# Kernel tuning notes

Hardware: AMD Instinct MI355X
Metric: run time of the kernel (lower is better)

The kernel has to match this reference:

```python
import jax, jax.numpy as jnp
import numpy as np

MARGIN = 0.3
EPS = 1e-12  # guards sqrt at zero distance (diagonal)


def setup_inputs() -> dict:
    key = jax.random.key(0)
    k1, k2 = jax.random.split(key)
    features = jax.random.normal(k1, (8192, 256), dtype=jnp.float32)
    labels = jax.random.randint(k2, (8192,), 0, 512, dtype=jnp.int64)
    return {"features": features, "labels": labels}


def reference(features, labels):
    # L2 normalize rows (F.normalize default: p=2, dim=1, eps=1e-12)
    norm = jnp.linalg.norm(features, axis=1, keepdims=True)
    f = features / jnp.maximum(norm, 1e-12)

    # pairwise euclidean distances: ||a||^2 + ||b||^2 - 2 a.b, then sqrt
    sq = jnp.sum(f * f, axis=1)  # [N]
    gram = f @ f.T               # [N, N]
    d2 = sq[:, None] + sq[None, :] - 2.0 * gram
    dist = jnp.sqrt(jnp.clip(d2, EPS))  # [N, N]

    mask_pos = labels[:, None] == labels[None, :]  # includes diagonal, as in torch code

    hardest_pos = jnp.max(dist * mask_pos.astype(dist.dtype), axis=1)
    dist_neg = jnp.where(mask_pos, jnp.inf, dist)
    hardest_neg = jnp.min(dist_neg, axis=1)

    loss = jax.nn.relu(hardest_pos - hardest_neg + MARGIN)
    return jnp.mean(loss)
```

## Files before the change

kernel.cpp:

```cpp
#include <hip/hip_runtime.h>
#include <hip/hip_bf16.h>
#include <hip/hip_fp8.h>
#include <math.h>

#define N 8192
#define D 256
#define MARGIN 0.3f
#define EPS 1e-12f

#define BT 128
#define NJB (N / BT)
#define TOTAL_TRI (NJB * (NJB + 1) / 2)

typedef __attribute__((ext_vector_type(4))) float floatx4;
typedef long long fp8x8;
typedef __attribute__((ext_vector_type(2))) long long llx2;

static __device__ inline unsigned char f2fp8(float f) {
    __hip_fp8_e4m3 h(f);
    return *reinterpret_cast<unsigned char*>(&h);
}


__global__ __launch_bounds__(256) void normalize_kernel(const float* __restrict__ x,
                                                        unsigned char* __restrict__ fn8t,
                                                        float* __restrict__ out) {
    __shared__ unsigned char lnorm[16][256];
    const int g    = blockIdx.x;
    const int t    = threadIdx.x;
    const int w    = t >> 6;
    const int lane = t & 63;
    if (g == 0 && t == 0) out[0] = 0.0f;

    #pragma unroll
    for (int rr = 0; rr < 4; rr++) {
        const int rl  = w * 4 + rr;
        const int row = g * 16 + rl;
        float4 v = ((const float4*)(x + (size_t)row * D))[lane];
        float s = v.x * v.x + v.y * v.y + v.z * v.z + v.w * v.w;
        #pragma unroll
        for (int off = 32; off; off >>= 1) s += __shfl_down(s, off);
        s = __shfl(s, 0);
        const float inv = 1.0f / fmaxf(sqrtf(s), 1e-12f);
        uchar4 b;
        b.x = f2fp8(v.x * inv); b.y = f2fp8(v.y * inv);
        b.z = f2fp8(v.z * inv); b.w = f2fp8(v.w * inv);
        *(uchar4*)(&lnorm[rl][lane * 4]) = b;
    }
    __syncthreads();
    const int kk = t >> 5;
    const int pp = (t & 31) * 2;
    unsigned char* base = fn8t + (size_t)g * 4096 + (kk >> 1) * 1024 + (kk & 1) * 8;
    #pragma unroll
    for (int e = 0; e < 2; e++) {
        const int p    = pp + e;
        const int quad = p >> 4;
        const int l15  = p & 15;
        *(fp8x8*)(base + p * 16) = *(const fp8x8*)(&lnorm[l15][kk * 32 + quad * 8]);
    }
}

__global__ __launch_bounds__(256, 3) void gram_kernel(const unsigned char* __restrict__ fn8t,
                                                      const int* __restrict__ lab,
                                                      float* __restrict__ gp_part,
                                                      float* __restrict__ gn_part) {
    __shared__ float rT[4][BT][17];
    __shared__ float cGp[BT][2], cGn[BT][2];

    const int bidx = blockIdx.x;
    const int idx  = (bidx & 7) * 260 + (bidx >> 3);
    const float c = 2.0f * NJB + 1.0f;
    int ib = (int)((c - sqrtf(c * c - 8.0f * (float)idx)) * 0.5f);
    while (ib > 0 && idx < ib * NJB - ib * (ib - 1) / 2) ib--;
    while (idx >= (ib + 1) * NJB - (ib + 1) * ib / 2) ib++;
    const int jb = ib + (idx - (ib * NJB - ib * (ib - 1) / 2));
    const bool offdiag = (jb > ib);
    const int i0 = ib * BT, j0 = jb * BT;

    const int t    = threadIdx.x;
    const int w    = t >> 6;
    const int lane = t & 63;
    const int wi   = w >> 1, wj = w & 1;
    const int quad = lane >> 4;
    const int l15  = lane & 15;

    const unsigned char* pA[4];
    const unsigned char* pB[4];
    #pragma unroll
    for (int m = 0; m < 4; m++)
        pA[m] = fn8t + ((size_t)(ib * 8 + wi * 4 + m)) * 4096 + lane * 16;
    #pragma unroll
    for (int n = 0; n < 4; n++)
        pB[n] = fn8t + ((size_t)(jb * 8 + wj * 4 + n)) * 4096 + lane * 16;

    floatx4 acc[4][4];
    #pragma unroll
    for (int m = 0; m < 4; m++)
        #pragma unroll
        for (int n = 0; n < 4; n++)
            acc[m][n] = (floatx4){0.f, 0.f, 0.f, 0.f};

    #pragma unroll
    for (int P = 0; P < 4; P++) {
        llx2 a2[4], b2[4];
        #pragma unroll
        for (int m = 0; m < 4; m++) a2[m] = *(const llx2*)(pA[m] + P * 1024);
        #pragma unroll
        for (int n = 0; n < 4; n++) b2[n] = *(const llx2*)(pB[n] + P * 1024);
        #pragma unroll
        for (int m = 0; m < 4; m++)
            #pragma unroll
            for (int n = 0; n < 4; n++)
                acc[m][n] = __builtin_amdgcn_mfma_f32_16x16x32_fp8_fp8(a2[m][0], b2[n][0], acc[m][n], 0, 0, 0);
        #pragma unroll
        for (int m = 0; m < 4; m++)
            #pragma unroll
            for (int n = 0; n < 4; n++)
                acc[m][n] = __builtin_amdgcn_mfma_f32_16x16x32_fp8_fp8(a2[m][1], b2[n][1], acc[m][n], 0, 0, 0);
    }

    int labj[4];
    #pragma unroll
    for (int n = 0; n < 4; n++) labj[n] = lab[j0 + wj * 64 + n * 16 + l15];
    float gpc[4], gnc[4];
    #pragma unroll
    for (int n = 0; n < 4; n++) { gpc[n] = INFINITY; gnc[n] = -INFINITY; }

    #pragma unroll
    for (int m = 0; m < 4; m++) {
        const int4 li4 = *(const int4*)(lab + i0 + wi * 64 + m * 16 + quad * 4);
        const int labi[4] = {li4.x, li4.y, li4.z, li4.w};
        #pragma unroll
        for (int r = 0; r < 4; r++) {
            float pr = INFINITY, nr = -INFINITY;
            #pragma unroll
            for (int n = 0; n < 4; n++) {
                const float g = acc[m][n][r];
                const bool same = (labi[r] == labj[n]);
                const float selp = same ? g : INFINITY;
                const float seln = same ? -INFINITY : g;
                pr = fminf(pr, selp);           nr = fmaxf(nr, seln);
                gpc[n] = fminf(gpc[n], selp);   gnc[n] = fmaxf(gnc[n], seln);
            }
            if (offdiag) {
                const int irow = wi * 64 + m * 16 + quad * 4 + r;
                rT[(wj << 1) + 0][irow][l15] = pr;
                rT[(wj << 1) + 1][irow][l15] = nr;
            }
        }
    }
    #pragma unroll
    for (int n = 0; n < 4; n++) {
        float p = gpc[n], q2 = gnc[n];
        p  = fminf(p,  __shfl_xor(p, 16));  p  = fminf(p,  __shfl_xor(p, 32));
        q2 = fmaxf(q2, __shfl_xor(q2, 16)); q2 = fmaxf(q2, __shfl_xor(q2, 32));
        if (quad == 0) {
            const int col = wj * 64 + n * 16 + l15;
            cGp[col][wi] = p; cGn[col][wi] = q2;
        }
    }
    __syncthreads();
    if (t < BT) {
        gp_part[(size_t)ib * N + j0 + t] = fminf(cGp[t][0], cGp[t][1]);
        gn_part[(size_t)ib * N + j0 + t] = fmaxf(cGn[t][0], cGn[t][1]);
    } else if (offdiag) {
        const int i = t - BT;
        float p = INFINITY, nn = -INFINITY;
        #pragma unroll
        for (int k = 0; k < 16; k++) {
            p  = fminf(p,  fminf(rT[0][i][k], rT[2][i][k]));
            nn = fmaxf(nn, fmaxf(rT[1][i][k], rT[3][i][k]));
        }
        gp_part[(size_t)jb * N + i0 + i] = p;
        gn_part[(size_t)jb * N + i0 + i] = nn;
    }
}

__global__ __launch_bounds__(256) void reduce_kernel(const float* __restrict__ gp_part,
                                                     const float* __restrict__ gn_part,
                                                     float* __restrict__ out) {
    __shared__ float redp[32][5], redn[32][5];
    const int t  = threadIdx.x;
    const int r  = blockIdx.x * 32 + (t & 31);
    const int sg = t >> 5;
    float gp = INFINITY, gn = -INFINITY;
    #pragma unroll
    for (int q = 0; q < 8; q++) {
        const int s = sg * 8 + q;
        gp = fminf(gp, gp_part[(size_t)s * N + r]);
        gn = fmaxf(gn, gn_part[(size_t)s * N + r]);
    }
    gp = fminf(gp, __shfl_xor(gp, 32));
    gn = fmaxf(gn, __shfl_xor(gn, 32));
    const int w = t >> 6;
    if ((t & 63) < 32) { redp[t & 31][w] = gp; redn[t & 31][w] = gn; }
    __syncthreads();
    if (t < 32) {
        const float p  = fminf(fminf(redp[t][0], redp[t][1]), fminf(redp[t][2], redp[t][3]));
        const float nn = fmaxf(fmaxf(redn[t][0], redn[t][1]), fmaxf(redn[t][2], redn[t][3]));
        const float dp = sqrtf(fmaxf(2.0f - 2.0f * p,  EPS));
        const float dn = sqrtf(fmaxf(2.0f - 2.0f * nn, EPS));
        const float l  = dp - dn + MARGIN;
        float sum = (l > 0.0f) ? l : 0.0f;
        #pragma unroll
        for (int off = 16; off; off >>= 1) sum += __shfl_down(sum, off);
        if (t == 0) atomicAdd(out, sum * (1.0f / (float)N));
    }
}

extern "C" void kernel_launch(void* const* d_in, const int* in_sizes, int n_in,
                              void* d_out, int out_size, void* d_ws, size_t ws_size,
                              hipStream_t stream) {
    const float* x   = (const float*)d_in[0];
    const int*   lab = (const int*)d_in[1];
    float* out = (float*)d_out;

    char* ws = (char*)d_ws;
    unsigned char* fn8t = (unsigned char*)ws;
    float* gp_part = (float*)(ws + (size_t)N * D);
    float* gn_part = gp_part + (size_t)NJB * N;

    normalize_kernel<<<N / 16, 256, 0, stream>>>(x, fn8t, out);
    gram_kernel<<<TOTAL_TRI, 256, 0, stream>>>(fn8t, lab, gp_part, gn_part);
    reduce_kernel<<<N / 32, 256, 0, stream>>>(gp_part, gn_part, out);
}
```

Baseline: 88.21 us.

## Switch gram kernel to 32x32x16 fp8 MFMA with matching fp8 layout

Replaces the 4x4 grid of 16x16x32 fp8 MFMA tiles per wave with a 2x2 grid of 32x32x16 MFMA tiles. The normalize kernel now writes the packed fp8 operands in a 32-row-group layout to match. The epilogue row/column reductions are reworked for the 32x32 accumulator layout, adding a shuffle before the shared-memory row writes. Launch bounds are raised to 4 blocks per SM to improve occupancy. The larger MFMA tile is meant to cut the number of operand loads and instructions per block, at the cost of a more complex epilogue.

```diff
diff --git a/kernel.cpp b/kernel.cpp
--- a/kernel.cpp
+++ b/kernel.cpp
@@ -12,7 +12,7 @@
 #define NJB (N / BT)
 #define TOTAL_TRI (NJB * (NJB + 1) / 2)
 
-typedef __attribute__((ext_vector_type(4))) float floatx4;
+typedef __attribute__((ext_vector_type(16))) float floatx16;
 typedef long long fp8x8;
 typedef __attribute__((ext_vector_type(2))) long long llx2;
 
@@ -25,17 +25,17 @@
 __global__ __launch_bounds__(256) void normalize_kernel(const float* __restrict__ x,
                                                         unsigned char* __restrict__ fn8t,
                                                         float* __restrict__ out) {
-    __shared__ unsigned char lnorm[16][256];
-    const int g    = blockIdx.x;
+    __shared__ unsigned char lnorm[32][256];
+    const int G    = blockIdx.x;
     const int t    = threadIdx.x;
     const int w    = t >> 6;
     const int lane = t & 63;
-    if (g == 0 && t == 0) out[0] = 0.0f;
-
-    #pragma unroll
-    for (int rr = 0; rr < 4; rr++) {
-        const int rl  = w * 4 + rr;
-        const int row = g * 16 + rl;
+    if (G == 0 && t == 0) out[0] = 0.0f;
+
+    #pragma unroll
+    for (int rr = 0; rr < 8; rr++) {
+        const int rl  = w * 8 + rr;
+        const int row = G * 32 + rl;
         float4 v = ((const float4*)(x + (size_t)row * D))[lane];
         float s = v.x * v.x + v.y * v.y + v.z * v.z + v.w * v.w;
         #pragma unroll
@@ -48,19 +48,17 @@
         *(uchar4*)(&lnorm[rl][lane * 4]) = b;
     }
     __syncthreads();
-    const int kk = t >> 5;
-    const int pp = (t & 31) * 2;
-    unsigned char* base = fn8t + (size_t)g * 4096 + (kk >> 1) * 1024 + (kk & 1) * 8;
-    #pragma unroll
-    for (int e = 0; e < 2; e++) {
-        const int p    = pp + e;
-        const int quad = p >> 4;
-        const int l15  = p & 15;
-        *(fp8x8*)(base + p * 16) = *(const fp8x8*)(&lnorm[l15][kk * 32 + quad * 8]);
-    }
-}
-
-__global__ __launch_bounds__(256, 3) void gram_kernel(const unsigned char* __restrict__ fn8t,
+    const int s  = t >> 4;
+    const int p0 = (t & 15) * 4;
+    unsigned char* base = fn8t + (size_t)G * 8192 + (s >> 1) * 1024 + (s & 1) * 8;
+    #pragma unroll
+    for (int e = 0; e < 4; e++) {
+        const int p = p0 + e;
+        *(fp8x8*)(base + p * 16) = *(const fp8x8*)(&lnorm[p & 31][s * 16 + (p >> 5) * 8]);
+    }
+}
+
+__global__ __launch_bounds__(256, 4) void gram_kernel(const unsigned char* __restrict__ fn8t,
                                                       const int* __restrict__ lab,
                                                       float* __restrict__ gp_part,
                                                       float* __restrict__ gn_part) {
@@ -81,81 +79,89 @@
     const int w    = t >> 6;
     const int lane = t & 63;
     const int wi   = w >> 1, wj = w & 1;
-    const int quad = lane >> 4;
-    const int l15  = lane & 15;
-
-    const unsigned char* pA[4];
-    const unsigned char* pB[4];
-    #pragma unroll
-    for (int m = 0; m < 4; m++)
-        pA[m] = fn8t + ((size_t)(ib * 8 + wi * 4 + m)) * 4096 + lane * 16;
-    #pragma unroll
-    for (int n = 0; n < 4; n++)
-        pB[n] = fn8t + ((size_t)(jb * 8 + wj * 4 + n)) * 4096 + lane * 16;
-
-    floatx4 acc[4][4];
-    #pragma unroll
-    for (int m = 0; m < 4; m++)
-        #pragma unroll
-        for (int n = 0; n < 4; n++)
-            acc[m][n] = (floatx4){0.f, 0.f, 0.f, 0.f};
-
-    #pragma unroll
-    for (int P = 0; P < 4; P++) {
-        llx2 a2[4], b2[4];
-        #pragma unroll
-        for (int m = 0; m < 4; m++) a2[m] = *(const llx2*)(pA[m] + P * 1024);
-        #pragma unroll
-        for (int n = 0; n < 4; n++) b2[n] = *(const llx2*)(pB[n] + P * 1024);
-        #pragma unroll
-        for (int m = 0; m < 4; m++)
+    const int l31  = lane & 31;
+    const int hi   = lane >> 5;
+
+    const unsigned char* pA[2];
+    const unsigned char* pB[2];
+    #pragma unroll
+    for (int m = 0; m < 2; m++)
+        pA[m] = fn8t + ((size_t)(ib * 4 + wi * 2 + m)) * 8192 + lane * 16;
+    #pragma unroll
+    for (int n = 0; n < 2; n++)
+        pB[n] = fn8t + ((size_t)(jb * 4 + wj * 2 + n)) * 8192 + lane * 16;
+
+    floatx16 acc[2][2];
+    #pragma unroll
+    for (int m = 0; m < 2; m++)
+        #pragma unroll
+        for (int n = 0; n < 2; n++)
+            acc[m][n] = (floatx16)(0.0f);
+
+    #pragma unroll
+    for (int P = 0; P < 8; P++) {
+        llx2 a2[2], b2[2];
+        #pragma unroll
+        for (int m = 0; m < 2; m++) a2[m] = *(const llx2*)(pA[m] + P * 1024);
+        #pragma unroll
+        for (int n = 0; n < 2; n++) b2[n] = *(const llx2*)(pB[n] + P * 1024);
+        #pragma unroll
+        for (int m = 0; m < 2; m++)
             #pragma unroll
-            for (int n = 0; n < 4; n++)
-                acc[m][n] = __builtin_amdgcn_mfma_f32_16x16x32_fp8_fp8(a2[m][0], b2[n][0], acc[m][n], 0, 0, 0);
-        #pragma unroll
-        for (int m = 0; m < 4; m++)
+            for (int n = 0; n < 2; n++)
+                acc[m][n] = __builtin_amdgcn_mfma_f32_32x32x16_fp8_fp8(a2[m][0], b2[n][0], acc[m][n], 0, 0, 0);
+        #pragma unroll
+        for (int m = 0; m < 2; m++)
             #pragma unroll
-            for (int n = 0; n < 4; n++)
-                acc[m][n] = __builtin_amdgcn_mfma_f32_16x16x32_fp8_fp8(a2[m][1], b2[n][1], acc[m][n], 0, 0, 0);
-    }
-
-    int labj[4];
-    #pragma unroll
-    for (int n = 0; n < 4; n++) labj[n] = lab[j0 + wj * 64 + n * 16 + l15];
-    float gpc[4], gnc[4];
-    #pragma unroll
-    for (int n = 0; n < 4; n++) { gpc[n] = INFINITY; gnc[n] = -INFINITY; }
-
-    #pragma unroll
-    for (int m = 0; m < 4; m++) {
-        const int4 li4 = *(const int4*)(lab + i0 + wi * 64 + m * 16 + quad * 4);
-        const int labi[4] = {li4.x, li4.y, li4.z, li4.w};
-        #pragma unroll
-        for (int r = 0; r < 4; r++) {
-            float pr = INFINITY, nr = -INFINITY;
+            for (int n = 0; n < 2; n++)
+                acc[m][n] = __builtin_amdgcn_mfma_f32_32x32x16_fp8_fp8(a2[m][1], b2[n][1], acc[m][n], 0, 0, 0);
+    }
+
+    int labj[2];
+    #pragma unroll
+    for (int n = 0; n < 2; n++) labj[n] = lab[j0 + wj * 64 + n * 32 + l31];
+    float gpc[2], gnc[2];
+    #pragma unroll
+    for (int n = 0; n < 2; n++) { gpc[n] = INFINITY; gnc[n] = -INFINITY; }
+
+    #pragma unroll
+    for (int m = 0; m < 2; m++) {
+        #pragma unroll
+        for (int q = 0; q < 4; q++) {
+            const int4 li4 = *(const int4*)(lab + i0 + wi * 64 + m * 32 + q * 8 + hi * 4);
+            const int labi[4] = {li4.x, li4.y, li4.z, li4.w};
             #pragma unroll
-            for (int n = 0; n < 4; n++) {
-                const float g = acc[m][n][r];
-                const bool same = (labi[r] == labj[n]);
-                const float selp = same ? g : INFINITY;
-                const float seln = same ? -INFINITY : g;
-                pr = fminf(pr, selp);           nr = fmaxf(nr, seln);
-                gpc[n] = fminf(gpc[n], selp);   gnc[n] = fmaxf(gnc[n], seln);
-            }
-            if (offdiag) {
-                const int irow = wi * 64 + m * 16 + quad * 4 + r;
-                rT[(wj << 1) + 0][irow][l15] = pr;
-                rT[(wj << 1) + 1][irow][l15] = nr;
+            for (int rr = 0; rr < 4; rr++) {
+                const int reg = q * 4 + rr;
+                float pr = INFINITY, nr = -INFINITY;
+                #pragma unroll
+                for (int n = 0; n < 2; n++) {
+                    const float g = acc[m][n][reg];
+                    const bool same = (labi[rr] == labj[n]);
+                    const float selp = same ? g : INFINITY;
+                    const float seln = same ? -INFINITY : g;
+                    pr = fminf(pr, selp);           nr = fmaxf(nr, seln);
+                    gpc[n] = fminf(gpc[n], selp);   gnc[n] = fmaxf(gnc[n], seln);
+                }
+                if (offdiag) {
+                    pr = fminf(pr, __shfl_xor(pr, 16));
+                    nr = fmaxf(nr, __shfl_xor(nr, 16));
+                    if (l31 < 16) {
+                        const int irow = wi * 64 + m * 32 + q * 8 + rr + hi * 4;
+                        rT[(wj << 1) + 0][irow][l31] = pr;
+                        rT[(wj << 1) + 1][irow][l31] = nr;
+                    }
+                }
             }
         }
     }
     #pragma unroll
-    for (int n = 0; n < 4; n++) {
+    for (int n = 0; n < 2; n++) {
         float p = gpc[n], q2 = gnc[n];
-        p  = fminf(p,  __shfl_xor(p, 16));  p  = fminf(p,  __shfl_xor(p, 32));
-        q2 = fmaxf(q2, __shfl_xor(q2, 16)); q2 = fmaxf(q2, __shfl_xor(q2, 32));
-        if (quad == 0) {
-            const int col = wj * 64 + n * 16 + l15;
+        p  = fminf(p,  __shfl_xor(p, 32));
+        q2 = fmaxf(q2, __shfl_xor(q2, 32));
+        if (hi == 0) {
+            const int col = wj * 64 + n * 32 + l31;
             cGp[col][wi] = p; cGn[col][wi] = q2;
         }
     }
@@ -220,7 +226,7 @@
     float* gp_part = (float*)(ws + (size_t)N * D);
     float* gn_part = gp_part + (size_t)NJB * N;
 
-    normalize_kernel<<<N / 16, 256, 0, stream>>>(x, fn8t, out);
+    normalize_kernel<<<N / 32, 256, 0, stream>>>(x, fn8t, out);
     gram_kernel<<<TOTAL_TRI, 256, 0, stream>>>(fn8t, lab, gp_part, gn_part);
     reduce_kernel<<<N / 32, 256, 0, stream>>>(gp_part, gn_part, out);
 }
```

Result: slower. 101.6 us (+15.2%).
